# Performance work log

Hardware: AMD Instinct MI355X
Metric: run time of the kernel (lower is better)

## Reference

```python
import jax, jax.numpy as jnp
import numpy as np

HIDDEN_DIM = 128
ATTN_DIM = 64
B, N = 2, 512

def setup_inputs() -> dict:
    key = jax.random.key(0)
    ks = jax.random.split(key, 8)
    s = 0.05
    return {
        "X":    jax.random.normal(ks[0], (B, N, HIDDEN_DIM), dtype=jnp.float32),
        "Wo":   jax.random.normal(ks[1], (ATTN_DIM, HIDDEN_DIM), dtype=jnp.float32) * s,
        "W1":   jax.random.normal(ks[2], (ATTN_DIM, HIDDEN_DIM), dtype=jnp.float32) * s,
        "Wphi": jax.random.normal(ks[3], (ATTN_DIM,), dtype=jnp.float32) * s,
        "Wy":   jax.random.normal(ks[4], (HIDDEN_DIM, HIDDEN_DIM), dtype=jnp.float32) * s,
        "by":   jax.random.normal(ks[5], (HIDDEN_DIM,), dtype=jnp.float32) * s,
        "We":   jax.random.normal(ks[6], (HIDDEN_DIM, ATTN_DIM), dtype=jnp.float32) * s,
        "be":   jax.random.normal(ks[7], (HIDDEN_DIM,), dtype=jnp.float32) * s,
    }

def reference(X, Wo, W1, Wphi, Wy, by, We, be):
    # h_o, h_1: [B, N, A]
    h_o = jnp.einsum('bnc,ac->bna', X, Wo)
    h_1 = jnp.einsum('bnc,ac->bna', X, W1)
    # pairwise tanh edge features e_ij: [B, N, N, A]
    e = jnp.tanh(h_o[:, :, None, :] + h_1[:, None, :, :])
    # scores [B, N, N] via w_phi projection, row-wise softmax over j
    scores = jnp.einsum('bija,a->bij', e, Wphi)
    alpha = jax.nn.softmax(scores, axis=-1)
    # value path 1: Wy x_j -> aggregated by alpha (bmm)
    X_y = jnp.einsum('bnc,hc->bnh', X, Wy) + by
    part1 = jnp.einsum('bij,bjh->bih', alpha, X_y)
    # value path 2: We e_ij -> weighted sum over j
    eval_ = jnp.einsum('bija,ha->bijh', e, We) + be  # [B, N, N, H]
    part2 = jnp.einsum('bij,bijh->bih', alpha, eval_)
    return part1 + part2
```

## Files before the change

### kernel.cpp

```cpp
#include <hip/hip_runtime.h>

#define B_ 2
#define N_ 512
#define C_ 128
#define A_ 64
#define H_ 128

#define SC2L 2.885390081777927f
#define LG2E 1.4426950408889634f

#define OFF_WOT 0
#define OFF_W1T (OFF_WOT + C_*A_)
#define OFF_WYT (OFF_W1T + C_*A_)
#define OFF_WET (OFF_WYT + C_*H_)
#define OFF_TO  (OFF_WET + A_*H_)
#define OFF_T1S (OFF_TO + B_*N_*A_)
#define OFF_T1T (OFF_T1S + B_*N_*A_)
#define OFF_XY  (OFF_T1T + B_*N_*A_)

__device__ __forceinline__ float fexp2(float x) { return __builtin_amdgcn_exp2f(x); }
__device__ __forceinline__ float frcp(float x)  { return __builtin_amdgcn_rcpf(x); }
__device__ __forceinline__ float ftanh(float x) {
  return 1.0f - 2.0f * frcp(fexp2(SC2L * x) + 1.0f);
}

__global__ __launch_bounds__(256) void prep_weights(
    const float* __restrict__ Wo, const float* __restrict__ W1,
    const float* __restrict__ Wy, const float* __restrict__ We,
    float* __restrict__ ws) {
  int t = blockIdx.x * 256 + threadIdx.x;
  if (t < A_*C_) {
    int a = t / C_, c = t % C_;
    ws[OFF_WOT + c*A_ + a] = Wo[t];
    ws[OFF_W1T + c*A_ + a] = W1[t];
    int h2 = t / A_, a2 = t % A_;
    ws[OFF_WET + a2*H_ + h2] = We[t];
  }
  if (t < H_*C_) {
    int h = t / C_, c = t % C_;
    ws[OFF_WYT + c*H_ + h] = Wy[t];
  }
}

__global__ __launch_bounds__(256) void proj_kernel(
    const float* __restrict__ X, const float* __restrict__ by,
    float* __restrict__ ws) {
  __shared__ float xs[2*C_];
  int row0 = blockIdx.x * 2;
  int t = threadIdx.x;
  if (t < 2*C_) xs[t] = X[(size_t)row0*C_ + t];
  __syncthreads();

  const float* wt;
  int col, stride;
  if (t < 64)       { wt = ws + OFF_WOT; col = t;       stride = A_; }
  else if (t < 128) { wt = ws + OFF_W1T; col = t - 64;  stride = A_; }
  else              { wt = ws + OFF_WYT; col = t - 128; stride = H_; }

  float acc0 = 0.f, acc1 = 0.f;
  #pragma unroll 8
  for (int c = 0; c < C_; ++c) {
    float wv = wt[c*stride + col];
    acc0 = fmaf(xs[c], wv, acc0);
    acc1 = fmaf(xs[C_ + c], wv, acc1);
  }
  if (t < 64) {
    float* o = ws + OFF_TO + (size_t)row0*A_ + col;
    o[0] = ftanh(acc0); o[A_] = ftanh(acc1);
  } else if (t < 128) {
    float t0 = ftanh(acc0), t1 = ftanh(acc1);
    float* o = ws + OFF_T1S + (size_t)row0*A_ + col;
    o[0] = t0; o[A_] = t1;
    int b = row0 >> 9, n0 = row0 & (N_-1);
    float* oT = ws + OFF_T1T + (size_t)b*A_*N_ + (size_t)col*N_ + n0;
    oT[0] = t0; oT[1] = t1;
  } else {
    float bb = by[col];
    float* o = ws + OFF_XY + (size_t)row0*H_ + col;
    o[0] = acc0 + bb; o[H_] = acc1 + bb;
  }
}

__global__ __launch_bounds__(512) void attn_kernel(
    const float* __restrict__ Wphi, const float* __restrict__ be,
    const float* __restrict__ ws, float* __restrict__ out) {
  __shared__ __align__(16) float4 pk[A_];
  __shared__ float tos[A_];
  __shared__ float sc[N_];
  __shared__ float reds[8];
  __shared__ float ebw[8][A_];
  __shared__ float ebar[A_];
  __shared__ float p1s[4][H_];

  int t = threadIdx.x;
  int w = t >> 6, lane = t & 63;
  int bi = blockIdx.x;
  int b = bi >> 9, i = bi & (N_-1);

  const float* t1s = ws + OFF_T1S + (size_t)(b*N_)*A_;
  const float* t1t = ws + OFF_T1T + (size_t)b*A_*N_;
  const float* xyg = ws + OFF_XY  + (size_t)(b*N_)*H_;
  const float* wet = ws + OFF_WET;

  if (t < A_) {
    float to = ws[OFF_TO + (size_t)(b*N_ + i)*A_ + t];
    float wv = Wphi[t];
    pk[t] = make_float4(to, wv*to, wv, 0.f);
    tos[t] = to;
  }
  __syncthreads();

  float s = 0.f;
  {
    const float* t1p = t1t + t;
    #pragma unroll 8
    for (int a = 0; a < A_; ++a) {
      float tb = t1p[(size_t)a*N_];
      float4 k = pk[a];
      float den = fmaf(k.x, tb, 1.0f);
      float num = fmaf(k.z, tb, k.y);
      s = fmaf(num, frcp(den), s);
    }
  }
  float p = fexp2(LG2E * s);
  sc[t] = p;
  float q = p;
  #pragma unroll
  for (int m = 1; m < 64; m <<= 1) q += __shfl_xor(q, m);
  if (lane == 0) reds[w] = q;
  __syncthreads();

  {
    float to = tos[lane];
    float c = 0.f;
    #pragma unroll 8
    for (int jj = 0; jj < N_/8; ++jj) {
      int j = jj*8 + w;
      float tb = t1s[(size_t)j*A_ + lane];
      float pj = sc[j];
      float den = fmaf(to, tb, 1.0f);
      c = fmaf(pj*(to + tb), frcp(den), c);
    }
    ebw[w][lane] = c;
  }

  {
    int h = t & 127, qd = t >> 7;
    const float* xq = xyg + (size_t)(qd*128)*H_ + h;
    float d = 0.f;
    #pragma unroll 8
    for (int jc = 0; jc < 128; ++jc) {
      d = fmaf(sc[qd*128 + jc], xq[(size_t)jc*H_], d);
    }
    p1s[qd][h] = d;
  }
  __syncthreads();

  if (t < A_) {
    float e = 0.f;
    #pragma unroll
    for (int k = 0; k < 8; ++k) e += ebw[k][t];
    ebar[t] = e;
  }
  __syncthreads();

  if (t < H_) {
    int h = t;
    float l = 0.f;
    #pragma unroll
    for (int k = 0; k < 8; ++k) l += reds[k];
    float acc = p1s[0][h] + p1s[1][h] + p1s[2][h] + p1s[3][h];
    float e2 = 0.f;
    #pragma unroll 8
    for (int a = 0; a < A_; ++a) e2 = fmaf(ebar[a], wet[a*H_ + h], e2);
    out[(size_t)bi*H_ + h] = (acc + e2) * frcp(l) + be[h];
  }
}

extern "C" void kernel_launch(void* const* d_in, const int* in_sizes, int n_in,
                              void* d_out, int out_size, void* d_ws, size_t ws_size,
                              hipStream_t stream) {
  const float* X    = (const float*)d_in[0];
  const float* Wo   = (const float*)d_in[1];
  const float* W1   = (const float*)d_in[2];
  const float* Wphi = (const float*)d_in[3];
  const float* Wy   = (const float*)d_in[4];
  const float* by   = (const float*)d_in[5];
  const float* We   = (const float*)d_in[6];
  const float* be   = (const float*)d_in[7];
  float* out = (float*)d_out;
  float* ws  = (float*)d_ws;

  hipLaunchKernelGGL(prep_weights, dim3(64), dim3(256), 0, stream, Wo, W1, Wy, We, ws);
  hipLaunchKernelGGL(proj_kernel, dim3(B_*N_/2), dim3(256), 0, stream, X, by, ws);
  hipLaunchKernelGGL(attn_kernel, dim3(B_*N_), dim3(512), 0, stream, Wphi, be, ws, out);
}
```

Baseline: 99.50 us.

## Reformulate tanh pair terms via exponentials and store intermediates as packed bf16

The tanh of a sum is rewritten in terms of per-token exponentials u=exp(2h1) and v=exp(2ho), so each pair term needs one fma and one reciprocal instead of tanh-addition algebra. The softmax score gets a constant offset that cancels, and the edge mean becomes l - 2*sum(p/(1+v*u)). The h1 exponentials and the Wy projection are stored as packed bf16 pairs, which halves the global/L2 traffic in the attention kernel. In exchange, bf16 rounding and the possible overflow of exponentials at large pre-activations reduce accuracy.

Result: faster. 94.56 us (-5.0%).

```diff
diff --git a/kernel.cpp b/kernel.cpp
--- a/kernel.cpp
+++ b/kernel.cpp
@@ -7,22 +7,25 @@
 #define H_ 128
 
 #define SC2L 2.885390081777927f
-#define LG2E 1.4426950408889634f
+#define NEG2LE -2.885390081777927f
 
 #define OFF_WOT 0
 #define OFF_W1T (OFF_WOT + C_*A_)
 #define OFF_WYT (OFF_W1T + C_*A_)
 #define OFF_WET (OFF_WYT + C_*H_)
-#define OFF_TO  (OFF_WET + A_*H_)
-#define OFF_T1S (OFF_TO + B_*N_*A_)
-#define OFF_T1T (OFF_T1S + B_*N_*A_)
-#define OFF_XY  (OFF_T1T + B_*N_*A_)
+#define OFF_V   (OFF_WET + A_*H_)
+#define OFF_UT2 (OFF_V   + B_*N_*A_)
+#define OFF_USP (OFF_UT2 + B_*N_*A_/2)
+#define OFF_XYP (OFF_USP + B_*N_*A_/2)
 
 __device__ __forceinline__ float fexp2(float x) { return __builtin_amdgcn_exp2f(x); }
 __device__ __forceinline__ float frcp(float x)  { return __builtin_amdgcn_rcpf(x); }
-__device__ __forceinline__ float ftanh(float x) {
-  return 1.0f - 2.0f * frcp(fexp2(SC2L * x) + 1.0f);
-}
+__device__ __forceinline__ unsigned f2bf(float x) {
+  unsigned u = __float_as_uint(x);
+  return (u + 0x7fffu + ((u >> 16) & 1u)) >> 16;
+}
+__device__ __forceinline__ float bf_lo(unsigned d) { return __uint_as_float(d << 16); }
+__device__ __forceinline__ float bf_hi(unsigned d) { return __uint_as_float(d & 0xffff0000u); }
 
 __global__ __launch_bounds__(256) void prep_weights(
     const float* __restrict__ Wo, const float* __restrict__ W1,
@@ -64,28 +67,38 @@
     acc0 = fmaf(xs[c], wv, acc0);
     acc1 = fmaf(xs[C_ + c], wv, acc1);
   }
+
+  int b = row0 >> 9, n0 = row0 & (N_-1);
+  int k = n0 >> 1;
+
   if (t < 64) {
-    float* o = ws + OFF_TO + (size_t)row0*A_ + col;
-    o[0] = ftanh(acc0); o[A_] = ftanh(acc1);
+    float* o = ws + OFF_V + (size_t)row0*A_ + col;
+    o[0] = fexp2(SC2L * acc0);
+    o[A_] = fexp2(SC2L * acc1);
   } else if (t < 128) {
-    float t0 = ftanh(acc0), t1 = ftanh(acc1);
-    float* o = ws + OFF_T1S + (size_t)row0*A_ + col;
-    o[0] = t0; o[A_] = t1;
-    int b = row0 >> 9, n0 = row0 & (N_-1);
-    float* oT = ws + OFF_T1T + (size_t)b*A_*N_ + (size_t)col*N_ + n0;
-    oT[0] = t0; oT[1] = t1;
+    int a = col;
+    unsigned u0 = f2bf(fexp2(SC2L * acc0));
+    unsigned u1 = f2bf(fexp2(SC2L * acc1));
+    unsigned* usp = (unsigned*)(ws + OFF_USP);
+    usp[(size_t)(b*(N_/2) + k)*A_ + a] = u0 | (u1 << 16);
+    unsigned short* ut = (unsigned short*)(ws + OFF_UT2);
+    size_t base = ((size_t)(b*(A_/2) + (a >> 1))*N_ + n0)*2 + (a & 1);
+    ut[base] = (unsigned short)u0;
+    ut[base + 2] = (unsigned short)u1;
   } else {
-    float bb = by[col];
-    float* o = ws + OFF_XY + (size_t)row0*H_ + col;
-    o[0] = acc0 + bb; o[H_] = acc1 + bb;
+    int h = col;
+    float bb = by[h];
+    unsigned x0 = f2bf(acc0 + bb);
+    unsigned x1 = f2bf(acc1 + bb);
+    unsigned* xp = (unsigned*)(ws + OFF_XYP);
+    xp[(size_t)(b*(N_/2) + k)*H_ + h] = x0 | (x1 << 16);
   }
 }
 
 __global__ __launch_bounds__(512) void attn_kernel(
     const float* __restrict__ Wphi, const float* __restrict__ be,
     const float* __restrict__ ws, float* __restrict__ out) {
-  __shared__ __align__(16) float4 pk[A_];
-  __shared__ float tos[A_];
+  __shared__ __align__(16) float2 pk2[A_];
   __shared__ float sc[N_];
   __shared__ float reds[8];
   __shared__ float ebw[8][A_];
@@ -97,32 +110,30 @@
   int bi = blockIdx.x;
   int b = bi >> 9, i = bi & (N_-1);
 
-  const float* t1s = ws + OFF_T1S + (size_t)(b*N_)*A_;
-  const float* t1t = ws + OFF_T1T + (size_t)b*A_*N_;
-  const float* xyg = ws + OFF_XY  + (size_t)(b*N_)*H_;
+  const unsigned* ut2 = (const unsigned*)(ws + OFF_UT2) + (size_t)b*(A_/2)*N_;
+  const unsigned* usp = (const unsigned*)(ws + OFF_USP) + (size_t)b*(N_/2)*A_;
+  const unsigned* xyp = (const unsigned*)(ws + OFF_XYP) + (size_t)b*(N_/2)*H_;
   const float* wet = ws + OFF_WET;
 
   if (t < A_) {
-    float to = ws[OFF_TO + (size_t)(b*N_ + i)*A_ + t];
-    float wv = Wphi[t];
-    pk[t] = make_float4(to, wv*to, wv, 0.f);
-    tos[t] = to;
+    pk2[t] = make_float2(ws[OFF_V + (size_t)(b*N_ + i)*A_ + t], Wphi[t]);
   }
   __syncthreads();
 
   float s = 0.f;
   {
-    const float* t1p = t1t + t;
-    #pragma unroll 8
-    for (int a = 0; a < A_; ++a) {
-      float tb = t1p[(size_t)a*N_];
-      float4 k = pk[a];
-      float den = fmaf(k.x, tb, 1.0f);
-      float num = fmaf(k.z, tb, k.y);
-      s = fmaf(num, frcp(den), s);
+    const unsigned* up = ut2 + t;
+    const float4* pkq = (const float4*)pk2;
+    #pragma unroll 8
+    for (int a2 = 0; a2 < A_/2; ++a2) {
+      unsigned d = up[(size_t)a2*N_];
+      float u0 = bf_lo(d), u1 = bf_hi(d);
+      float4 vw = pkq[a2];
+      s = fmaf(vw.y, frcp(fmaf(vw.x, u0, 1.f)), s);
+      s = fmaf(vw.w, frcp(fmaf(vw.z, u1, 1.f)), s);
     }
   }
-  float p = fexp2(LG2E * s);
+  float p = fexp2(NEG2LE * s);
   sc[t] = p;
   float q = p;
   #pragma unroll
@@ -131,28 +142,33 @@
   __syncthreads();
 
   {
-    float to = tos[lane];
+    float v = pk2[lane].x;
+    const unsigned* up = usp + lane;
     float c = 0.f;
     #pragma unroll 8
-    for (int jj = 0; jj < N_/8; ++jj) {
-      int j = jj*8 + w;
-      float tb = t1s[(size_t)j*A_ + lane];
-      float pj = sc[j];
-      float den = fmaf(to, tb, 1.0f);
-      c = fmaf(pj*(to + tb), frcp(den), c);
+    for (int kk = 0; kk < N_/16; ++kk) {
+      int k = kk*8 + w;
+      unsigned d = up[(size_t)k*A_];
+      float u0 = bf_lo(d), u1 = bf_hi(d);
+      float p0 = sc[2*k], p1 = sc[2*k + 1];
+      c = fmaf(p0, frcp(fmaf(v, u0, 1.f)), c);
+      c = fmaf(p1, frcp(fmaf(v, u1, 1.f)), c);
     }
     ebw[w][lane] = c;
   }
 
   {
     int h = t & 127, qd = t >> 7;
-    const float* xq = xyg + (size_t)(qd*128)*H_ + h;
-    float d = 0.f;
-    #pragma unroll 8
-    for (int jc = 0; jc < 128; ++jc) {
-      d = fmaf(sc[qd*128 + jc], xq[(size_t)jc*H_], d);
+    const unsigned* xp = xyp + (size_t)(qd*64)*H_ + h;
+    float d0 = 0.f;
+    #pragma unroll 8
+    for (int kc = 0; kc < 64; ++kc) {
+      unsigned d = xp[(size_t)kc*H_];
+      int j = (qd*64 + kc)*2;
+      d0 = fmaf(sc[j],     bf_lo(d), d0);
+      d0 = fmaf(sc[j + 1], bf_hi(d), d0);
     }
-    p1s[qd][h] = d;
+    p1s[qd][h] = d0;
   }
   __syncthreads();
 
@@ -160,7 +176,10 @@
     float e = 0.f;
     #pragma unroll
     for (int k = 0; k < 8; ++k) e += ebw[k][t];
-    ebar[t] = e;
+    float l = 0.f;
+    #pragma unroll
+    for (int k = 0; k < 8; ++k) l += reds[k];
+    ebar[t] = l - 2.0f*e;
   }
   __syncthreads();
 
```
